# Kernel tuning notes

Measured on AMD Instinct MI355X. Metric: run time of the kernel, lower is better.

## Reference

```python
import jax, jax.numpy as jnp
import numpy as np

N = 50_000          # nodes
E = 1_600_000       # edges (avg degree 32)
F_IN = 8            # num_static_node_features
F_OUT = 12          # num_timesteps_in (TGCN hidden)
PERIODS = 6         # num_timesteps_out


def setup_inputs() -> dict:
    key = jax.random.key(0)
    ks = jax.random.split(key, 12)
    def n(k, shape, s=0.2):
        return jax.random.normal(k, shape, jnp.float32) * s
    return {
        "x": jax.random.normal(ks[0], (N, F_IN, PERIODS), jnp.float32),
        "edge_index": jax.random.randint(ks[1], (2, E), 0, N, dtype=jnp.int32),
        "edge_weight": jax.random.uniform(ks[2], (E,), jnp.float32),
        "att": n(ks[3], (PERIODS,), 1.0),
        "Wz": n(ks[4], (F_IN, F_OUT)), "bz": jnp.zeros((F_OUT,), jnp.float32),
        "Wr": n(ks[5], (F_IN, F_OUT)), "br": jnp.zeros((F_OUT,), jnp.float32),
        "Wh": n(ks[6], (F_IN, F_OUT)), "bh": jnp.zeros((F_OUT,), jnp.float32),
        "lzW": n(ks[7], (F_OUT, 2 * F_OUT)), "lzb": jnp.zeros((F_OUT,), jnp.float32),
        "lrW": n(ks[8], (F_OUT, 2 * F_OUT)), "lrb": jnp.zeros((F_OUT,), jnp.float32),
        "lhW": n(ks[9], (F_OUT, 2 * F_OUT)), "lhb": jnp.zeros((F_OUT,), jnp.float32),
        "linW": n(ks[10], (PERIODS, F_OUT)), "linb": jnp.zeros((PERIODS,), jnp.float32),
    }


def _gcn_norm(edge_index, edge_weight):
    # PyG gcn_norm: add self loops (weight 1.0), symmetric D^-1/2 A D^-1/2,
    # degree computed from dst (col) of edge_weight.
    src, dst = edge_index[0], edge_index[1]
    loop = jnp.arange(N, dtype=src.dtype)
    src = jnp.concatenate([src, loop])
    dst = jnp.concatenate([dst, loop])
    ew = jnp.concatenate([edge_weight, jnp.ones((N,), edge_weight.dtype)])
    deg = jax.ops.segment_sum(ew, dst, num_segments=N)
    dinv = jnp.where(deg > 0, 1.0 / jnp.sqrt(deg), 0.0)
    return src, dst, dinv[src] * ew * dinv[dst]


def _gcn_conv(xp, W, b, src, dst, norm):
    h = xp @ W                                  # [N, F_OUT]
    msg = norm[:, None] * h[src]                # gather over edges
    return jax.ops.segment_sum(msg, dst, num_segments=N) + b


def reference(x, edge_index, edge_weight, att, Wz, bz, Wr, br, Wh, bh,
              lzW, lzb, lrW, lrb, lhW, lhb, linW, linb):
    src, dst, norm = _gcn_norm(edge_index, edge_weight)
    H0 = jnp.zeros((N, F_OUT), x.dtype)  # A3TGCN passes H=None each period

    def tgcn_cell(xp):  # xp: [N, F_IN]
        Z = jax.nn.sigmoid(
            jnp.concatenate([_gcn_conv(xp, Wz, bz, src, dst, norm), H0], -1) @ lzW.T + lzb)
        R = jax.nn.sigmoid(
            jnp.concatenate([_gcn_conv(xp, Wr, br, src, dst, norm), H0], -1) @ lrW.T + lrb)
        Ht = jnp.tanh(
            jnp.concatenate([_gcn_conv(xp, Wh, bh, src, dst, norm), H0 * R], -1) @ lhW.T + lhb)
        return Z * H0 + (1.0 - Z) * Ht

    probs = jax.nn.softmax(att)                  # [P]
    Hs = jax.vmap(tgcn_cell, in_axes=2)(x)       # [P, N, F_OUT]
    H = jnp.einsum('p,pnf->nf', probs, Hs)       # attention-weighted sum
    h = jax.nn.relu(H)
    return h @ linW.T + linb                     # [N, PERIODS]
```

## Files before the change

### kernel.cpp

```cpp
#include <hip/hip_runtime.h>
#include <hip/hip_fp16.h>

#define N_NODES 50000
#define N_EDGES 1600000
#define F_IN 8
#define F_OUT 12
#define PERIODS 6
#define FP 48
#define BKT_SH 7
#define BKT_N 128
#define NBKT ((N_NODES + BKT_N - 1) / BKT_N)
#define CHK 4096
#define NCHK ((N_EDGES + CHK - 1) / CHK)
#define SEG_CAP 4736
#define SEG_AL  5120

typedef unsigned int u32x4 __attribute__((ext_vector_type(4)));

__global__ void k_zero(unsigned int* __restrict__ cursor) {
    int i = threadIdx.x;
    if (i < NBKT) cursor[i] = 0u;
}

__global__ void __launch_bounds__(1024) k_scatter(const int4* __restrict__ src4,
                                                  const int4* __restrict__ dst4,
                                                  const float4* __restrict__ ew4,
                                                  unsigned int* __restrict__ cursor,
                                                  unsigned long long* __restrict__ part) {
    __shared__ unsigned int h[NBKT];
    __shared__ unsigned int gbase[NBKT];
    int tid = threadIdx.x, blk = blockIdx.x;
    for (int k = tid; k < NBKT; k += 1024) h[k] = 0u;
    __syncthreads();
    int q = blk * 1024 + tid;
    bool v = (q < N_EDGES / 4);
    int4 ss = v ? src4[q] : make_int4(0, 0, 0, 0);
    int4 dd = v ? dst4[q] : make_int4(0, 0, 0, 0);
    float4 ww = v ? ew4[q] : make_float4(0.f, 0.f, 0.f, 0.f);
    int s[4] = { ss.x, ss.y, ss.z, ss.w };
    int d[4] = { dd.x, dd.y, dd.z, dd.w };
    float w[4] = { ww.x, ww.y, ww.z, ww.w };
    int bv[4]; unsigned int lr[4], lo[4], hiw[4];
    #pragma unroll
    for (int e = 0; e < 4; e++) {
        if (v) {
            int b = d[e] >> BKT_SH;
            bv[e] = b;
            lr[e] = atomicAdd(&h[b], 1u);
            lo[e] = ((unsigned int)(d[e] & (BKT_N - 1)) << 24) | (unsigned int)s[e];
            hiw[e] = __float_as_uint(w[e]);
        }
    }
    __syncthreads();
    for (int k = tid; k < NBKT; k += 1024) {
        unsigned int c = h[k];
        gbase[k] = c ? atomicAdd(&cursor[k], c) : 0u;
    }
    __syncthreads();
    if (v) {
        #pragma unroll
        for (int e = 0; e < 4; e++) {
            unsigned int off = gbase[bv[e]] + lr[e];
            if (off < SEG_CAP)
                part[(size_t)bv[e] * SEG_CAP + off] =
                    ((unsigned long long)hiw[e] << 32) | lo[e];
        }
    }
}

__global__ void __launch_bounds__(1024) k_bucket(const unsigned long long* __restrict__ part,
                                                 const unsigned int* __restrict__ cursor,
                                                 const float* __restrict__ x,
                                                 int2* __restrict__ offs2,
                                                 float* __restrict__ dinv_g,
                                                 uint4* __restrict__ xs,
                                                 unsigned int* __restrict__ csr4) {
    __shared__ uint2 stage[SEG_CAP];
    __shared__ unsigned int cnt[BKT_N], rowstart[BKT_N], sc[BKT_N];
    __shared__ float degf[BKT_N], dinv_l[BKT_N];
    int tid = threadIdx.x, k = blockIdx.x;
    unsigned int base = (unsigned int)k * SEG_CAP;
    unsigned int cbase = (unsigned int)k * SEG_AL;
    unsigned int m = cursor[k];
    if (m > SEG_CAP) m = SEG_CAP;
    if (tid < BKT_N) { cnt[tid] = 0u; degf[tid] = 1.0f; }
    __syncthreads();

    for (unsigned int i = tid; i < m; i += 1024) {
        unsigned long long p = __builtin_nontemporal_load(&part[base + i]);
        unsigned int lo = (unsigned int)p;
        unsigned int hi = (unsigned int)(p >> 32);
        unsigned int j = (lo >> 24) & (BKT_N - 1);
        unsigned int r = atomicAdd(&cnt[j], 1u);
        atomicAdd(&degf[j], __uint_as_float(hi));
        if (r > 255u) r = 255u;
        stage[i] = make_uint2(lo | (r << 16), hi);
    }
    __syncthreads();

    if (tid < 64) {
        unsigned int a = (cnt[tid] + 3u) & ~3u;
        unsigned int b = (cnt[tid + 64] + 3u) & ~3u;
        unsigned int sa = a;
        #pragma unroll
        for (int off = 1; off < 64; off <<= 1) {
            unsigned int tv = __shfl_up(sa, off);
            if ((tid & 63) >= off) sa += tv;
        }
        unsigned int tot = __shfl(sa, 63);
        unsigned int sb = b;
        #pragma unroll
        for (int off = 1; off < 64; off <<= 1) {
            unsigned int tv = __shfl_up(sb, off);
            if ((tid & 63) >= off) sb += tv;
        }
        sc[tid] = sa;
        sc[tid + 64] = sb + tot;
    }
    __syncthreads();

    int n0 = k * BKT_N;
    int nn = N_NODES - n0; if (nn > BKT_N) nn = BKT_N;

    if (tid < BKT_N) {
        unsigned int ca = (cnt[tid] + 3u) & ~3u;
        unsigned int rs = sc[tid] - ca;
        rowstart[tid] = rs;
        float dv = rsqrtf(degf[tid]);
        dinv_l[tid] = dv;
        if (tid < nn) {
            dinv_g[n0 + tid] = dv;
            offs2[n0 + tid] = make_int2((int)(cbase + rs),
                                        (int)(cbase + rs + cnt[tid]));
        }
    }
    __syncthreads();

    for (unsigned int i = tid; i < m; i += 1024) {
        uint2 vv = stage[i];
        unsigned int j = (vv.x >> 24) & (BKT_N - 1);
        unsigned int r = (vv.x >> 16) & 0xFFu;
        __half hw = __float2half(__uint_as_float(vv.y));
        unsigned int entry = ((unsigned int)__half_as_ushort(hw) << 16) |
                             (vv.x & 0xFFFFu);
        csr4[cbase + rowstart[j] + r] = entry;
    }

    for (int idx = tid; idx < nn * 6; idx += 1024) {
        int j = idx / 6, c = idx % 6;
        float di = dinv_l[j];
        const float4* xr = (const float4*)(x + (size_t)(n0 + j) * FP + c * 8);
        float4 a = xr[0], b = xr[1];
        __half2 h0 = __floats2half2_rn(di * a.x, di * a.y);
        __half2 h1 = __floats2half2_rn(di * a.z, di * a.w);
        __half2 h2 = __floats2half2_rn(di * b.x, di * b.y);
        __half2 h3 = __floats2half2_rn(di * b.z, di * b.w);
        uint4 o;
        o.x = *(unsigned int*)&h0; o.y = *(unsigned int*)&h1;
        o.z = *(unsigned int*)&h2; o.w = *(unsigned int*)&h3;
        xs[(size_t)(n0 + j) * 6 + c] = o;
    }
}

__global__ void __launch_bounds__(192) k_gnode(const uint4* __restrict__ xs,
                                               const float* __restrict__ dinv,
                                               const int2* __restrict__ offs2,
                                               const unsigned int* __restrict__ csr4,
                                               const float* __restrict__ att,
                                               const float* __restrict__ Wz,
                                               const float* __restrict__ bz,
                                               const float* __restrict__ Wh,
                                               const float* __restrict__ bh,
                                               const float* __restrict__ lzW,
                                               const float* __restrict__ lzb,
                                               const float* __restrict__ lhW,
                                               const float* __restrict__ lhb,
                                               const float* __restrict__ linW,
                                               const float* __restrict__ linb,
                                               float* __restrict__ out) {
    __shared__ float row[8][48];
    __shared__ float gzs[8][72];
    __shared__ float ghs[8][72];
    __shared__ float Hl[8][12];

    int tid = threadIdx.x;
    int L = tid / 24, r = tid % 24, c = r >> 2, g = r & 3;
    int n = blockIdx.x * 8 + L;

    int2 oe = offs2[n];
    const unsigned int* rowp = csr4 + oe.x;
    int cnt = oe.y - oe.x;
    float a0 = 0.f, a1 = 0.f, a2 = 0.f, a3 = 0.f;
    float a4 = 0.f, a5 = 0.f, a6 = 0.f, a7 = 0.f;
    int kk = 0;
    for (; kk + 16 <= cnt; kk += 16) {
        u32x4 pc = __builtin_nontemporal_load((const u32x4*)(rowp + kk + 4 * g));
        unsigned int p[4] = { pc.x, pc.y, pc.z, pc.w };
        uint4 v[4];
        #pragma unroll
        for (int u = 0; u < 4; u++)
            v[u] = xs[(size_t)(p[u] & 0xFFFFu) * 6 + c];
        #pragma unroll
        for (int u = 0; u < 4; u++) {
            float w = __half2float(__ushort_as_half((unsigned short)(p[u] >> 16)));
            float2 e0 = __half22float2(*(__half2*)&v[u].x);
            float2 e1 = __half22float2(*(__half2*)&v[u].y);
            float2 e2 = __half22float2(*(__half2*)&v[u].z);
            float2 e3 = __half22float2(*(__half2*)&v[u].w);
            a0 += w * e0.x; a1 += w * e0.y; a2 += w * e1.x; a3 += w * e1.y;
            a4 += w * e2.x; a5 += w * e2.y; a6 += w * e3.x; a7 += w * e3.y;
        }
    }
    int tlo = kk + 4 * g, thi = tlo + 4; if (thi > cnt) thi = cnt;
    for (int jj = tlo; jj < thi; jj++) {
        unsigned int p = __builtin_nontemporal_load(rowp + jj);
        float w = __half2float(__ushort_as_half((unsigned short)(p >> 16)));
        uint4 v = xs[(size_t)(p & 0xFFFFu) * 6 + c];
        float2 e0 = __half22float2(*(__half2*)&v.x);
        float2 e1 = __half22float2(*(__half2*)&v.y);
        float2 e2 = __half22float2(*(__half2*)&v.z);
        float2 e3 = __half22float2(*(__half2*)&v.w);
        a0 += w * e0.x; a1 += w * e0.y; a2 += w * e1.x; a3 += w * e1.y;
        a4 += w * e2.x; a5 += w * e2.y; a6 += w * e3.x; a7 += w * e3.y;
    }
    a0 += __shfl_xor(a0, 1); a1 += __shfl_xor(a1, 1);
    a2 += __shfl_xor(a2, 1); a3 += __shfl_xor(a3, 1);
    a4 += __shfl_xor(a4, 1); a5 += __shfl_xor(a5, 1);
    a6 += __shfl_xor(a6, 1); a7 += __shfl_xor(a7, 1);
    a0 += __shfl_xor(a0, 2); a1 += __shfl_xor(a1, 2);
    a2 += __shfl_xor(a2, 2); a3 += __shfl_xor(a3, 2);
    a4 += __shfl_xor(a4, 2); a5 += __shfl_xor(a5, 2);
    a6 += __shfl_xor(a6, 2); a7 += __shfl_xor(a7, 2);
    if (g == 0) {
        uint4 sf = xs[(size_t)n * 6 + c];
        float2 s0 = __half22float2(*(__half2*)&sf.x);
        float2 s1 = __half22float2(*(__half2*)&sf.y);
        float2 s2 = __half22float2(*(__half2*)&sf.z);
        float2 s3 = __half22float2(*(__half2*)&sf.w);
        float di = dinv[n];
        row[L][8 * c + 0] = di * (a0 + s0.x); row[L][8 * c + 1] = di * (a1 + s0.y);
        row[L][8 * c + 2] = di * (a2 + s1.x); row[L][8 * c + 3] = di * (a3 + s1.y);
        row[L][8 * c + 4] = di * (a4 + s2.x); row[L][8 * c + 5] = di * (a5 + s2.y);
        row[L][8 * c + 6] = di * (a6 + s3.x); row[L][8 * c + 7] = di * (a7 + s3.y);
    }
    __syncthreads();

    for (int it = r; it < 72; it += 24) {
        int p = it / 12, q = it - p * 12;
        float gz = bz[q], gh = bh[q];
        #pragma unroll
        for (int f = 0; f < F_IN; f++) {
            float xv = row[L][f * 6 + p];
            gz += xv * Wz[f * F_OUT + q];
            gh += xv * Wh[f * F_OUT + q];
        }
        gzs[L][it] = gz; ghs[L][it] = gh;
    }
    __syncthreads();

    if (r < 12) {
        float a[PERIODS];
        float mx = -1e30f;
        #pragma unroll
        for (int p = 0; p < PERIODS; p++) { a[p] = att[p]; mx = fmaxf(mx, a[p]); }
        float se = 0.f;
        #pragma unroll
        for (int p = 0; p < PERIODS; p++) { a[p] = __expf(a[p] - mx); se += a[p]; }
        float inv = 1.f / se;
        int j = r;
        float hacc = 0.f;
        #pragma unroll
        for (int p = 0; p < PERIODS; p++) {
            float z = lzb[j], t2 = lhb[j];
            #pragma unroll
            for (int q = 0; q < F_OUT; q++) {
                z  += gzs[L][p * 12 + q] * lzW[j * (2 * F_OUT) + q];
                t2 += ghs[L][p * 12 + q] * lhW[j * (2 * F_OUT) + q];
            }
            float Z = 1.f / (1.f + __expf(-z));
            float e2 = __expf(2.f * t2);
            float th = 1.f - __fdividef(2.f, e2 + 1.f);
            hacc += (a[p] * inv) * (1.f - Z) * th;
        }
        Hl[L][j] = fmaxf(hacc, 0.f);
    }
    __syncthreads();

    if (r < PERIODS) {
        float acc = linb[r];
        #pragma unroll
        for (int j = 0; j < F_OUT; j++)
            acc += Hl[L][j] * linW[r * F_OUT + j];
        out[(size_t)n * PERIODS + r] = acc;
    }
}

extern "C" void kernel_launch(void* const* d_in, const int* in_sizes, int n_in,
                              void* d_out, int out_size, void* d_ws, size_t ws_size,
                              hipStream_t stream) {
    const float* x    = (const float*)d_in[0];
    const int*   ei   = (const int*)d_in[1];
    const float* ew   = (const float*)d_in[2];
    const float* att  = (const float*)d_in[3];
    const float* Wz   = (const float*)d_in[4];
    const float* bz   = (const float*)d_in[5];
    const float* Wh   = (const float*)d_in[8];
    const float* bh   = (const float*)d_in[9];
    const float* lzW  = (const float*)d_in[10];
    const float* lzb  = (const float*)d_in[11];
    const float* lhW  = (const float*)d_in[14];
    const float* lhb  = (const float*)d_in[15];
    const float* linW = (const float*)d_in[16];
    const float* linb = (const float*)d_in[17];
    float* out = (float*)d_out;

    uint4* xs   = (uint4*)d_ws;
    unsigned long long* part = (unsigned long long*)(xs + (size_t)N_NODES * 6);
    unsigned int* csr4 = (unsigned int*)(part + (size_t)NBKT * SEG_CAP);
    int2*  offs2 = (int2*)(csr4 + (size_t)NBKT * SEG_AL);
    float* dinv  = (float*)(offs2 + N_NODES);
    unsigned int* cursor = (unsigned int*)(dinv + N_NODES);

    const int* srcp = ei;
    const int* dstp = ei + N_EDGES;

    k_zero<<<1, 512, 0, stream>>>(cursor);
    k_scatter<<<NCHK, 1024, 0, stream>>>((const int4*)srcp, (const int4*)dstp,
                                         (const float4*)ew, cursor, part);
    k_bucket<<<NBKT, 1024, 0, stream>>>(part, cursor, x, offs2, dinv, xs, csr4);
    k_gnode<<<N_NODES / 8, 192, 0, stream>>>(xs, dinv, offs2, csr4, att,
                                             Wz, bz, Wh, bh, lzW, lzb, lhW, lhb,
                                             linW, linb, out);
}
```

Baseline: 187.3 us.

## Replace CSR build with per-bucket LDS atomic aggregation fused with node epilogue

Drops the per-bucket CSR construction and the separate per-node gather kernel. Each bucket block now reads its partitioned edges directly and accumulates weighted neighbour features into shared memory with atomics, then runs the GRU/attention/linear epilogue for its 128 nodes in the same kernel. Degree is accumulated with global float atomics in the scatter kernel, and a small kernel builds the scaled half-precision features. The aim is to remove the CSR write/read pass and one launch. In exchange it adds heavy LDS atomic traffic (48 per edge), global atomics on degree, and only about 391 blocks for the main work.

```diff
diff --git a/kernel.cpp b/kernel.cpp
--- a/kernel.cpp
+++ b/kernel.cpp
@@ -13,19 +13,19 @@
 #define CHK 4096
 #define NCHK ((N_EDGES + CHK - 1) / CHK)
 #define SEG_CAP 4736
-#define SEG_AL  5120
-
-typedef unsigned int u32x4 __attribute__((ext_vector_type(4)));
-
-__global__ void k_zero(unsigned int* __restrict__ cursor) {
-    int i = threadIdx.x;
-    if (i < NBKT) cursor[i] = 0u;
+#define ACC_W 49
+
+__global__ void k_init(unsigned int* __restrict__ cursor, float* __restrict__ deg) {
+    int t = blockIdx.x * blockDim.x + threadIdx.x;
+    if (t < N_NODES) deg[t] = 1.0f;
+    if (t < NBKT) cursor[t] = 0u;
 }
 
 __global__ void __launch_bounds__(1024) k_scatter(const int4* __restrict__ src4,
                                                   const int4* __restrict__ dst4,
                                                   const float4* __restrict__ ew4,
                                                   unsigned int* __restrict__ cursor,
+                                                  float* __restrict__ deg,
                                                   unsigned long long* __restrict__ part) {
     __shared__ unsigned int h[NBKT];
     __shared__ unsigned int gbase[NBKT];
@@ -49,6 +49,7 @@
             lr[e] = atomicAdd(&h[b], 1u);
             lo[e] = ((unsigned int)(d[e] & (BKT_N - 1)) << 24) | (unsigned int)s[e];
             hiw[e] = __float_as_uint(w[e]);
+            atomicAdd(&deg[d[e]], w[e]);
         }
     }
     __syncthreads();
@@ -68,230 +69,161 @@
     }
 }
 
-__global__ void __launch_bounds__(1024) k_bucket(const unsigned long long* __restrict__ part,
-                                                 const unsigned int* __restrict__ cursor,
-                                                 const float* __restrict__ x,
-                                                 int2* __restrict__ offs2,
-                                                 float* __restrict__ dinv_g,
-                                                 uint4* __restrict__ xs,
-                                                 unsigned int* __restrict__ csr4) {
-    __shared__ uint2 stage[SEG_CAP];
-    __shared__ unsigned int cnt[BKT_N], rowstart[BKT_N], sc[BKT_N];
-    __shared__ float degf[BKT_N], dinv_l[BKT_N];
+__global__ void __launch_bounds__(256) k_xs(const float* __restrict__ x,
+                                            const float* __restrict__ deg,
+                                            float* __restrict__ dinv,
+                                            uint4* __restrict__ xs) {
+    int t = blockIdx.x * 256 + threadIdx.x;
+    if (t >= N_NODES * 6) return;
+    int n = t / 6, c = t % 6;
+    float di = rsqrtf(deg[n]);
+    if (c == 0) dinv[n] = di;
+    const float4* xr = (const float4*)(x + (size_t)n * FP + c * 8);
+    float4 a = xr[0], b = xr[1];
+    __half2 h0 = __floats2half2_rn(di * a.x, di * a.y);
+    __half2 h1 = __floats2half2_rn(di * a.z, di * a.w);
+    __half2 h2 = __floats2half2_rn(di * b.x, di * b.y);
+    __half2 h3 = __floats2half2_rn(di * b.z, di * b.w);
+    uint4 o;
+    o.x = *(unsigned int*)&h0; o.y = *(unsigned int*)&h1;
+    o.z = *(unsigned int*)&h2; o.w = *(unsigned int*)&h3;
+    xs[t] = o;
+}
+
+__global__ void __launch_bounds__(1024) k_bedge(const unsigned long long* __restrict__ part,
+                                                const unsigned int* __restrict__ cursor,
+                                                const uint4* __restrict__ xs,
+                                                const float* __restrict__ dinv,
+                                                const float* __restrict__ att,
+                                                const float* __restrict__ Wz,
+                                                const float* __restrict__ bz,
+                                                const float* __restrict__ Wh,
+                                                const float* __restrict__ bh,
+                                                const float* __restrict__ lzW,
+                                                const float* __restrict__ lzb,
+                                                const float* __restrict__ lhW,
+                                                const float* __restrict__ lhb,
+                                                const float* __restrict__ linW,
+                                                const float* __restrict__ linb,
+                                                float* __restrict__ out) {
+    __shared__ float acc[BKT_N * ACC_W];
+    __shared__ float Hl[BKT_N * F_OUT];
+    __shared__ float dinv_l[BKT_N];
+
     int tid = threadIdx.x, k = blockIdx.x;
+    int n0 = k * BKT_N;
+    int nn = N_NODES - n0; if (nn > BKT_N) nn = BKT_N;
     unsigned int base = (unsigned int)k * SEG_CAP;
-    unsigned int cbase = (unsigned int)k * SEG_AL;
     unsigned int m = cursor[k];
     if (m > SEG_CAP) m = SEG_CAP;
-    if (tid < BKT_N) { cnt[tid] = 0u; degf[tid] = 1.0f; }
-    __syncthreads();
-
-    for (unsigned int i = tid; i < m; i += 1024) {
-        unsigned long long p = __builtin_nontemporal_load(&part[base + i]);
-        unsigned int lo = (unsigned int)p;
-        unsigned int hi = (unsigned int)(p >> 32);
-        unsigned int j = (lo >> 24) & (BKT_N - 1);
-        unsigned int r = atomicAdd(&cnt[j], 1u);
-        atomicAdd(&degf[j], __uint_as_float(hi));
-        if (r > 255u) r = 255u;
-        stage[i] = make_uint2(lo | (r << 16), hi);
-    }
-    __syncthreads();
-
-    if (tid < 64) {
-        unsigned int a = (cnt[tid] + 3u) & ~3u;
-        unsigned int b = (cnt[tid + 64] + 3u) & ~3u;
-        unsigned int sa = a;
-        #pragma unroll
-        for (int off = 1; off < 64; off <<= 1) {
-            unsigned int tv = __shfl_up(sa, off);
-            if ((tid & 63) >= off) sa += tv;
-        }
-        unsigned int tot = __shfl(sa, 63);
-        unsigned int sb = b;
-        #pragma unroll
-        for (int off = 1; off < 64; off <<= 1) {
-            unsigned int tv = __shfl_up(sb, off);
-            if ((tid & 63) >= off) sb += tv;
-        }
-        sc[tid] = sa;
-        sc[tid + 64] = sb + tot;
-    }
-    __syncthreads();
-
-    int n0 = k * BKT_N;
-    int nn = N_NODES - n0; if (nn > BKT_N) nn = BKT_N;
-
-    if (tid < BKT_N) {
-        unsigned int ca = (cnt[tid] + 3u) & ~3u;
-        unsigned int rs = sc[tid] - ca;
-        rowstart[tid] = rs;
-        float dv = rsqrtf(degf[tid]);
-        dinv_l[tid] = dv;
-        if (tid < nn) {
-            dinv_g[n0 + tid] = dv;
-            offs2[n0 + tid] = make_int2((int)(cbase + rs),
-                                        (int)(cbase + rs + cnt[tid]));
-        }
-    }
-    __syncthreads();
-
-    for (unsigned int i = tid; i < m; i += 1024) {
-        uint2 vv = stage[i];
-        unsigned int j = (vv.x >> 24) & (BKT_N - 1);
-        unsigned int r = (vv.x >> 16) & 0xFFu;
-        __half hw = __float2half(__uint_as_float(vv.y));
-        unsigned int entry = ((unsigned int)__half_as_ushort(hw) << 16) |
-                             (vv.x & 0xFFFFu);
-        csr4[cbase + rowstart[j] + r] = entry;
-    }
-
-    for (int idx = tid; idx < nn * 6; idx += 1024) {
-        int j = idx / 6, c = idx % 6;
-        float di = dinv_l[j];
-        const float4* xr = (const float4*)(x + (size_t)(n0 + j) * FP + c * 8);
-        float4 a = xr[0], b = xr[1];
-        __half2 h0 = __floats2half2_rn(di * a.x, di * a.y);
-        __half2 h1 = __floats2half2_rn(di * a.z, di * a.w);
-        __half2 h2 = __floats2half2_rn(di * b.x, di * b.y);
-        __half2 h3 = __floats2half2_rn(di * b.z, di * b.w);
-        uint4 o;
-        o.x = *(unsigned int*)&h0; o.y = *(unsigned int*)&h1;
-        o.z = *(unsigned int*)&h2; o.w = *(unsigned int*)&h3;
-        xs[(size_t)(n0 + j) * 6 + c] = o;
-    }
-}
-
-__global__ void __launch_bounds__(192) k_gnode(const uint4* __restrict__ xs,
-                                               const float* __restrict__ dinv,
-                                               const int2* __restrict__ offs2,
-                                               const unsigned int* __restrict__ csr4,
-                                               const float* __restrict__ att,
-                                               const float* __restrict__ Wz,
-                                               const float* __restrict__ bz,
-                                               const float* __restrict__ Wh,
-                                               const float* __restrict__ bh,
-                                               const float* __restrict__ lzW,
-                                               const float* __restrict__ lzb,
-                                               const float* __restrict__ lhW,
-                                               const float* __restrict__ lhb,
-                                               const float* __restrict__ linW,
-                                               const float* __restrict__ linb,
-                                               float* __restrict__ out) {
-    __shared__ float row[8][48];
-    __shared__ float gzs[8][72];
-    __shared__ float ghs[8][72];
-    __shared__ float Hl[8][12];
-
-    int tid = threadIdx.x;
-    int L = tid / 24, r = tid % 24, c = r >> 2, g = r & 3;
-    int n = blockIdx.x * 8 + L;
-
-    int2 oe = offs2[n];
-    const unsigned int* rowp = csr4 + oe.x;
-    int cnt = oe.y - oe.x;
-    float a0 = 0.f, a1 = 0.f, a2 = 0.f, a3 = 0.f;
-    float a4 = 0.f, a5 = 0.f, a6 = 0.f, a7 = 0.f;
-    int kk = 0;
-    for (; kk + 16 <= cnt; kk += 16) {
-        u32x4 pc = __builtin_nontemporal_load((const u32x4*)(rowp + kk + 4 * g));
-        unsigned int p[4] = { pc.x, pc.y, pc.z, pc.w };
-        uint4 v[4];
-        #pragma unroll
-        for (int u = 0; u < 4; u++)
-            v[u] = xs[(size_t)(p[u] & 0xFFFFu) * 6 + c];
-        #pragma unroll
-        for (int u = 0; u < 4; u++) {
-            float w = __half2float(__ushort_as_half((unsigned short)(p[u] >> 16)));
-            float2 e0 = __half22float2(*(__half2*)&v[u].x);
-            float2 e1 = __half22float2(*(__half2*)&v[u].y);
-            float2 e2 = __half22float2(*(__half2*)&v[u].z);
-            float2 e3 = __half22float2(*(__half2*)&v[u].w);
-            a0 += w * e0.x; a1 += w * e0.y; a2 += w * e1.x; a3 += w * e1.y;
-            a4 += w * e2.x; a5 += w * e2.y; a6 += w * e3.x; a7 += w * e3.y;
-        }
-    }
-    int tlo = kk + 4 * g, thi = tlo + 4; if (thi > cnt) thi = cnt;
-    for (int jj = tlo; jj < thi; jj++) {
-        unsigned int p = __builtin_nontemporal_load(rowp + jj);
-        float w = __half2float(__ushort_as_half((unsigned short)(p >> 16)));
-        uint4 v = xs[(size_t)(p & 0xFFFFu) * 6 + c];
-        float2 e0 = __half22float2(*(__half2*)&v.x);
-        float2 e1 = __half22float2(*(__half2*)&v.y);
-        float2 e2 = __half22float2(*(__half2*)&v.z);
-        float2 e3 = __half22float2(*(__half2*)&v.w);
-        a0 += w * e0.x; a1 += w * e0.y; a2 += w * e1.x; a3 += w * e1.y;
-        a4 += w * e2.x; a5 += w * e2.y; a6 += w * e3.x; a7 += w * e3.y;
-    }
-    a0 += __shfl_xor(a0, 1); a1 += __shfl_xor(a1, 1);
-    a2 += __shfl_xor(a2, 1); a3 += __shfl_xor(a3, 1);
-    a4 += __shfl_xor(a4, 1); a5 += __shfl_xor(a5, 1);
-    a6 += __shfl_xor(a6, 1); a7 += __shfl_xor(a7, 1);
-    a0 += __shfl_xor(a0, 2); a1 += __shfl_xor(a1, 2);
-    a2 += __shfl_xor(a2, 2); a3 += __shfl_xor(a3, 2);
-    a4 += __shfl_xor(a4, 2); a5 += __shfl_xor(a5, 2);
-    a6 += __shfl_xor(a6, 2); a7 += __shfl_xor(a7, 2);
-    if (g == 0) {
-        uint4 sf = xs[(size_t)n * 6 + c];
-        float2 s0 = __half22float2(*(__half2*)&sf.x);
-        float2 s1 = __half22float2(*(__half2*)&sf.y);
-        float2 s2 = __half22float2(*(__half2*)&sf.z);
-        float2 s3 = __half22float2(*(__half2*)&sf.w);
-        float di = dinv[n];
-        row[L][8 * c + 0] = di * (a0 + s0.x); row[L][8 * c + 1] = di * (a1 + s0.y);
-        row[L][8 * c + 2] = di * (a2 + s1.x); row[L][8 * c + 3] = di * (a3 + s1.y);
-        row[L][8 * c + 4] = di * (a4 + s2.x); row[L][8 * c + 5] = di * (a5 + s2.y);
-        row[L][8 * c + 6] = di * (a6 + s3.x); row[L][8 * c + 7] = di * (a7 + s3.y);
-    }
-    __syncthreads();
-
-    for (int it = r; it < 72; it += 24) {
-        int p = it / 12, q = it - p * 12;
-        float gz = bz[q], gh = bh[q];
-        #pragma unroll
-        for (int f = 0; f < F_IN; f++) {
-            float xv = row[L][f * 6 + p];
-            gz += xv * Wz[f * F_OUT + q];
-            gh += xv * Wh[f * F_OUT + q];
-        }
-        gzs[L][it] = gz; ghs[L][it] = gh;
-    }
-    __syncthreads();
-
-    if (r < 12) {
-        float a[PERIODS];
-        float mx = -1e30f;
-        #pragma unroll
-        for (int p = 0; p < PERIODS; p++) { a[p] = att[p]; mx = fmaxf(mx, a[p]); }
-        float se = 0.f;
-        #pragma unroll
-        for (int p = 0; p < PERIODS; p++) { a[p] = __expf(a[p] - mx); se += a[p]; }
-        float inv = 1.f / se;
-        int j = r;
-        float hacc = 0.f;
-        #pragma unroll
-        for (int p = 0; p < PERIODS; p++) {
-            float z = lzb[j], t2 = lhb[j];
-            #pragma unroll
-            for (int q = 0; q < F_OUT; q++) {
-                z  += gzs[L][p * 12 + q] * lzW[j * (2 * F_OUT) + q];
-                t2 += ghs[L][p * 12 + q] * lhW[j * (2 * F_OUT) + q];
-            }
-            float Z = 1.f / (1.f + __expf(-z));
-            float e2 = __expf(2.f * t2);
-            float th = 1.f - __fdividef(2.f, e2 + 1.f);
-            hacc += (a[p] * inv) * (1.f - Z) * th;
-        }
-        Hl[L][j] = fmaxf(hacc, 0.f);
-    }
-    __syncthreads();
-
-    if (r < PERIODS) {
-        float acc = linb[r];
-        #pragma unroll
-        for (int j = 0; j < F_OUT; j++)
-            acc += Hl[L][j] * linW[r * F_OUT + j];
-        out[(size_t)n * PERIODS + r] = acc;
+
+    for (int i = tid; i < BKT_N * ACC_W; i += 1024) acc[i] = 0.f;
+    for (int i = tid; i < BKT_N * F_OUT; i += 1024) Hl[i] = 0.f;
+    if (tid < nn) dinv_l[tid] = dinv[n0 + tid];
+    __syncthreads();
+
+    {
+        int grp = tid >> 1, kk = tid & 1;
+        for (unsigned int e = grp; e < m; e += 512) {
+            unsigned long long pe = __builtin_nontemporal_load(&part[base + e]);
+            unsigned int lo = (unsigned int)pe;
+            float w = __uint_as_float((unsigned int)(pe >> 32));
+            int src = (int)(lo & 0xFFFFu);
+            int dl  = (int)((lo >> 24) & (BKT_N - 1));
+            float* arow = acc + dl * ACC_W;
+            #pragma unroll
+            for (int u = 0; u < 3; u++) {
+                int c = kk + 2 * u;
+                uint4 vv = xs[(size_t)src * 6 + c];
+                float2 e0 = __half22float2(*(__half2*)&vv.x);
+                float2 e1 = __half22float2(*(__half2*)&vv.y);
+                float2 e2 = __half22float2(*(__half2*)&vv.z);
+                float2 e3 = __half22float2(*(__half2*)&vv.w);
+                float* ap = arow + 8 * c;
+                atomicAdd(&ap[0], w * e0.x); atomicAdd(&ap[1], w * e0.y);
+                atomicAdd(&ap[2], w * e1.x); atomicAdd(&ap[3], w * e1.y);
+                atomicAdd(&ap[4], w * e2.x); atomicAdd(&ap[5], w * e2.y);
+                atomicAdd(&ap[6], w * e3.x); atomicAdd(&ap[7], w * e3.y);
+            }
+        }
+    }
+    __syncthreads();
+
+    if (tid < BKT_N * 6) {
+        int j = tid / 6, c = tid % 6;
+        if (j < nn) {
+            uint4 vv = xs[(size_t)(n0 + j) * 6 + c];
+            float dv = dinv_l[j];
+            float2 e0 = __half22float2(*(__half2*)&vv.x);
+            float2 e1 = __half22float2(*(__half2*)&vv.y);
+            float2 e2 = __half22float2(*(__half2*)&vv.z);
+            float2 e3 = __half22float2(*(__half2*)&vv.w);
+            float* ap = acc + j * ACC_W + 8 * c;
+            ap[0] = dv * (ap[0] + e0.x); ap[1] = dv * (ap[1] + e0.y);
+            ap[2] = dv * (ap[2] + e1.x); ap[3] = dv * (ap[3] + e1.y);
+            ap[4] = dv * (ap[4] + e2.x); ap[5] = dv * (ap[5] + e2.y);
+            ap[6] = dv * (ap[6] + e3.x); ap[7] = dv * (ap[7] + e3.y);
+        }
+    }
+    __syncthreads();
+
+    if (tid < PERIODS * BKT_N) {
+        int p = tid >> 7, jn = tid & (BKT_N - 1);
+        if (jn < nn) {
+            float mx = -1e30f;
+            #pragma unroll
+            for (int pp = 0; pp < PERIODS; pp++) mx = fmaxf(mx, att[pp]);
+            float se = 0.f, ap = 0.f;
+            #pragma unroll
+            for (int pp = 0; pp < PERIODS; pp++) {
+                float ev = __expf(att[pp] - mx);
+                se += ev;
+                if (pp == p) ap = ev;
+            }
+            ap /= se;
+
+            float rv[F_IN];
+            #pragma unroll
+            for (int f = 0; f < F_IN; f++) rv[f] = acc[jn * ACC_W + f * 6 + p];
+
+            float gz[F_OUT], gh[F_OUT];
+            #pragma unroll
+            for (int q = 0; q < F_OUT; q++) { gz[q] = bz[q]; gh[q] = bh[q]; }
+            #pragma unroll
+            for (int f = 0; f < F_IN; f++) {
+                float xv = rv[f];
+                #pragma unroll
+                for (int q = 0; q < F_OUT; q++) {
+                    gz[q] += xv * Wz[f * F_OUT + q];
+                    gh[q] += xv * Wh[f * F_OUT + q];
+                }
+            }
+            #pragma unroll
+            for (int j = 0; j < F_OUT; j++) {
+                float z = lzb[j], t2 = lhb[j];
+                #pragma unroll
+                for (int q = 0; q < F_OUT; q++) {
+                    z  += gz[q] * lzW[j * (2 * F_OUT) + q];
+                    t2 += gh[q] * lhW[j * (2 * F_OUT) + q];
+                }
+                float Z = 1.f / (1.f + __expf(-z));
+                float e2 = __expf(2.f * t2);
+                float th = 1.f - __fdividef(2.f, e2 + 1.f);
+                atomicAdd(&Hl[jn * F_OUT + j], ap * (1.f - Z) * th);
+            }
+        }
+    }
+    __syncthreads();
+
+    if (tid < BKT_N * PERIODS) {
+        int jn = tid / PERIODS, q = tid % PERIODS;
+        if (jn < nn) {
+            float a2 = linb[q];
+            #pragma unroll
+            for (int j = 0; j < F_OUT; j++)
+                a2 += fmaxf(Hl[jn * F_OUT + j], 0.f) * linW[q * F_OUT + j];
+            out[(size_t)(n0 + jn) * PERIODS + q] = a2;
+        }
     }
 }
 
@@ -316,19 +248,18 @@
 
     uint4* xs   = (uint4*)d_ws;
     unsigned long long* part = (unsigned long long*)(xs + (size_t)N_NODES * 6);
-    unsigned int* csr4 = (unsigned int*)(part + (size_t)NBKT * SEG_CAP);
-    int2*  offs2 = (int2*)(csr4 + (size_t)NBKT * SEG_AL);
-    float* dinv  = (float*)(offs2 + N_NODES);
+    float* deg  = (float*)(part + (size_t)NBKT * SEG_CAP);
+    float* dinv = deg + N_NODES;
     unsigned int* cursor = (unsigned int*)(dinv + N_NODES);
 
     const int* srcp = ei;
     const int* dstp = ei + N_EDGES;
 
-    k_zero<<<1, 512, 0, stream>>>(cursor);
+    k_init<<<(N_NODES + 1023) / 1024, 1024, 0, stream>>>(cursor, deg);
     k_scatter<<<NCHK, 1024, 0, stream>>>((const int4*)srcp, (const int4*)dstp,
-                                         (const float4*)ew, cursor, part);
-    k_bucket<<<NBKT, 1024, 0, stream>>>(part, cursor, x, offs2, dinv, xs, csr4);
-    k_gnode<<<N_NODES / 8, 192, 0, stream>>>(xs, dinv, offs2, csr4, att,
-                                             Wz, bz, Wh, bh, lzW, lzb, lhW, lhb,
-                                             linW, linb, out);
-}
+                                         (const float4*)ew, cursor, deg, part);
+    k_xs<<<(N_NODES * 6 + 255) / 256, 256, 0, stream>>>(x, deg, dinv, xs);
+    k_bedge<<<NBKT, 1024, 0, stream>>>(part, cursor, xs, dinv, att,
+                                       Wz, bz, Wh, bh, lzW, lzb, lhW, lhb,
+                                       linW, linb, out);
+}
```

After: 731.7 us. 291% more time.

## Fuse CSR bucket build with neighbor gather and move degree to scatter atomics

Applied to the files above, without the earlier changes.

Degree accumulation moves out of the bucket kernel into global fixed-point atomics during the edge scatter. A new elementwise kernel then computes dinv and the scaled half-precision node features up front. The bucket kernel is merged with the per-node gather and GRU/attention epilogue, so each 128-node bucket builds its CSR segment in LDS and consumes it immediately. This removes the offs2 array and one launch, but it costs 1.6M random global atomics, a large LDS footprint, and only ~391 blocks doing the latency-bound gather.

```diff
diff --git a/kernel.cpp b/kernel.cpp
--- a/kernel.cpp
+++ b/kernel.cpp
@@ -14,18 +14,22 @@
 #define NCHK ((N_EDGES + CHK - 1) / CHK)
 #define SEG_CAP 4736
 #define SEG_AL  5120
+#define DEG_SCALE 16777216.0f
+#define DEG_INV  5.9604644775390625e-8f
 
 typedef unsigned int u32x4 __attribute__((ext_vector_type(4)));
 
-__global__ void k_zero(unsigned int* __restrict__ cursor) {
-    int i = threadIdx.x;
-    if (i < NBKT) cursor[i] = 0u;
+__global__ void k_init(unsigned int* __restrict__ cursor, unsigned int* __restrict__ degu) {
+    int t = blockIdx.x * blockDim.x + threadIdx.x;
+    if (t < N_NODES) degu[t] = 1u << 24;
+    if (t < NBKT) cursor[t] = 0u;
 }
 
 __global__ void __launch_bounds__(1024) k_scatter(const int4* __restrict__ src4,
                                                   const int4* __restrict__ dst4,
                                                   const float4* __restrict__ ew4,
                                                   unsigned int* __restrict__ cursor,
+                                                  unsigned int* __restrict__ degu,
                                                   unsigned long long* __restrict__ part) {
     __shared__ unsigned int h[NBKT];
     __shared__ unsigned int gbase[NBKT];
@@ -49,6 +53,7 @@
             lr[e] = atomicAdd(&h[b], 1u);
             lo[e] = ((unsigned int)(d[e] & (BKT_N - 1)) << 24) | (unsigned int)s[e];
             hiw[e] = __float_as_uint(w[e]);
+            atomicAdd(&degu[d[e]], __float2uint_rn(w[e] * DEG_SCALE));
         }
     }
     __syncthreads();
@@ -68,22 +73,66 @@
     }
 }
 
-__global__ void __launch_bounds__(1024) k_bucket(const unsigned long long* __restrict__ part,
-                                                 const unsigned int* __restrict__ cursor,
-                                                 const float* __restrict__ x,
-                                                 int2* __restrict__ offs2,
-                                                 float* __restrict__ dinv_g,
-                                                 uint4* __restrict__ xs,
-                                                 unsigned int* __restrict__ csr4) {
-    __shared__ uint2 stage[SEG_CAP];
+__global__ void __launch_bounds__(256) k_xs(const float* __restrict__ x,
+                                            const unsigned int* __restrict__ degu,
+                                            float* __restrict__ dinv,
+                                            uint4* __restrict__ xs) {
+    int t = blockIdx.x * 256 + threadIdx.x;
+    if (t >= N_NODES * 6) return;
+    int n = t / 6, c = t % 6;
+    float di = rsqrtf((float)degu[n] * DEG_INV);
+    if (c == 0) dinv[n] = di;
+    const float4* xr = (const float4*)(x + (size_t)n * FP + c * 8);
+    float4 a = xr[0], b = xr[1];
+    __half2 h0 = __floats2half2_rn(di * a.x, di * a.y);
+    __half2 h1 = __floats2half2_rn(di * a.z, di * a.w);
+    __half2 h2 = __floats2half2_rn(di * b.x, di * b.y);
+    __half2 h3 = __floats2half2_rn(di * b.z, di * b.w);
+    uint4 o;
+    o.x = *(unsigned int*)&h0; o.y = *(unsigned int*)&h1;
+    o.z = *(unsigned int*)&h2; o.w = *(unsigned int*)&h3;
+    xs[t] = o;
+}
+
+__global__ void __launch_bounds__(1024) k_bgn(const unsigned long long* __restrict__ part,
+                                              const unsigned int* __restrict__ cursor,
+                                              const uint4* __restrict__ xs,
+                                              const float* __restrict__ dinv,
+                                              unsigned int* __restrict__ csr4,
+                                              const float* __restrict__ att,
+                                              const float* __restrict__ Wz,
+                                              const float* __restrict__ bz,
+                                              const float* __restrict__ Wh,
+                                              const float* __restrict__ bh,
+                                              const float* __restrict__ lzW,
+                                              const float* __restrict__ lzb,
+                                              const float* __restrict__ lhW,
+                                              const float* __restrict__ lhb,
+                                              const float* __restrict__ linW,
+                                              const float* __restrict__ linb,
+                                              float* __restrict__ out) {
+    __shared__ union {
+        uint2 stage[SEG_CAP];
+        struct {
+            float row[BKT_N][48];
+            float Hl[BKT_N][F_OUT];
+        } e;
+    } u;
+    __shared__ float gzs[64][72], ghs[64][72];
     __shared__ unsigned int cnt[BKT_N], rowstart[BKT_N], sc[BKT_N];
-    __shared__ float degf[BKT_N], dinv_l[BKT_N];
+    __shared__ float dinv_l[BKT_N];
+
     int tid = threadIdx.x, k = blockIdx.x;
+    int n0 = k * BKT_N;
+    int nn = N_NODES - n0; if (nn > BKT_N) nn = BKT_N;
     unsigned int base = (unsigned int)k * SEG_CAP;
     unsigned int cbase = (unsigned int)k * SEG_AL;
     unsigned int m = cursor[k];
     if (m > SEG_CAP) m = SEG_CAP;
-    if (tid < BKT_N) { cnt[tid] = 0u; degf[tid] = 1.0f; }
+    if (tid < BKT_N) {
+        cnt[tid] = 0u;
+        dinv_l[tid] = (tid < nn) ? dinv[n0 + tid] : 0.f;
+    }
     __syncthreads();
 
     for (unsigned int i = tid; i < m; i += 1024) {
@@ -92,9 +141,8 @@
         unsigned int hi = (unsigned int)(p >> 32);
         unsigned int j = (lo >> 24) & (BKT_N - 1);
         unsigned int r = atomicAdd(&cnt[j], 1u);
-        atomicAdd(&degf[j], __uint_as_float(hi));
         if (r > 255u) r = 255u;
-        stage[i] = make_uint2(lo | (r << 16), hi);
+        u.stage[i] = make_uint2(lo | (r << 16), hi);
     }
     __syncthreads();
 
@@ -118,26 +166,14 @@
         sc[tid + 64] = sb + tot;
     }
     __syncthreads();
-
-    int n0 = k * BKT_N;
-    int nn = N_NODES - n0; if (nn > BKT_N) nn = BKT_N;
-
     if (tid < BKT_N) {
         unsigned int ca = (cnt[tid] + 3u) & ~3u;
-        unsigned int rs = sc[tid] - ca;
-        rowstart[tid] = rs;
-        float dv = rsqrtf(degf[tid]);
-        dinv_l[tid] = dv;
-        if (tid < nn) {
-            dinv_g[n0 + tid] = dv;
-            offs2[n0 + tid] = make_int2((int)(cbase + rs),
-                                        (int)(cbase + rs + cnt[tid]));
-        }
+        rowstart[tid] = sc[tid] - ca;
     }
     __syncthreads();
 
     for (unsigned int i = tid; i < m; i += 1024) {
-        uint2 vv = stage[i];
+        uint2 vv = u.stage[i];
         unsigned int j = (vv.x >> 24) & (BKT_N - 1);
         unsigned int r = (vv.x >> 16) & 0xFFu;
         __half hw = __float2half(__uint_as_float(vv.y));
@@ -145,153 +181,126 @@
                              (vv.x & 0xFFFFu);
         csr4[cbase + rowstart[j] + r] = entry;
     }
-
-    for (int idx = tid; idx < nn * 6; idx += 1024) {
-        int j = idx / 6, c = idx % 6;
-        float di = dinv_l[j];
-        const float4* xr = (const float4*)(x + (size_t)(n0 + j) * FP + c * 8);
-        float4 a = xr[0], b = xr[1];
-        __half2 h0 = __floats2half2_rn(di * a.x, di * a.y);
-        __half2 h1 = __floats2half2_rn(di * a.z, di * a.w);
-        __half2 h2 = __floats2half2_rn(di * b.x, di * b.y);
-        __half2 h3 = __floats2half2_rn(di * b.z, di * b.w);
-        uint4 o;
-        o.x = *(unsigned int*)&h0; o.y = *(unsigned int*)&h1;
-        o.z = *(unsigned int*)&h2; o.w = *(unsigned int*)&h3;
-        xs[(size_t)(n0 + j) * 6 + c] = o;
-    }
-}
-
-__global__ void __launch_bounds__(192) k_gnode(const uint4* __restrict__ xs,
-                                               const float* __restrict__ dinv,
-                                               const int2* __restrict__ offs2,
-                                               const unsigned int* __restrict__ csr4,
-                                               const float* __restrict__ att,
-                                               const float* __restrict__ Wz,
-                                               const float* __restrict__ bz,
-                                               const float* __restrict__ Wh,
-                                               const float* __restrict__ bh,
-                                               const float* __restrict__ lzW,
-                                               const float* __restrict__ lzb,
-                                               const float* __restrict__ lhW,
-                                               const float* __restrict__ lhb,
-                                               const float* __restrict__ linW,
-                                               const float* __restrict__ linb,
-                                               float* __restrict__ out) {
-    __shared__ float row[8][48];
-    __shared__ float gzs[8][72];
-    __shared__ float ghs[8][72];
-    __shared__ float Hl[8][12];
-
-    int tid = threadIdx.x;
-    int L = tid / 24, r = tid % 24, c = r >> 2, g = r & 3;
-    int n = blockIdx.x * 8 + L;
-
-    int2 oe = offs2[n];
-    const unsigned int* rowp = csr4 + oe.x;
-    int cnt = oe.y - oe.x;
-    float a0 = 0.f, a1 = 0.f, a2 = 0.f, a3 = 0.f;
-    float a4 = 0.f, a5 = 0.f, a6 = 0.f, a7 = 0.f;
-    int kk = 0;
-    for (; kk + 16 <= cnt; kk += 16) {
-        u32x4 pc = __builtin_nontemporal_load((const u32x4*)(rowp + kk + 4 * g));
-        unsigned int p[4] = { pc.x, pc.y, pc.z, pc.w };
-        uint4 v[4];
-        #pragma unroll
-        for (int u = 0; u < 4; u++)
-            v[u] = xs[(size_t)(p[u] & 0xFFFFu) * 6 + c];
-        #pragma unroll
-        for (int u = 0; u < 4; u++) {
-            float w = __half2float(__ushort_as_half((unsigned short)(p[u] >> 16)));
-            float2 e0 = __half22float2(*(__half2*)&v[u].x);
-            float2 e1 = __half22float2(*(__half2*)&v[u].y);
-            float2 e2 = __half22float2(*(__half2*)&v[u].z);
-            float2 e3 = __half22float2(*(__half2*)&v[u].w);
+    __syncthreads();
+
+    for (int P = 0; P < 3; P++) {
+        int rr = P * 1024 + tid;
+        int nL = rr / 24, lane = rr % 24, c = lane >> 2, g = lane & 3;
+        const unsigned int* rowp = csr4 + cbase + rowstart[nL];
+        int cntv = (int)cnt[nL];
+        float a0 = 0.f, a1 = 0.f, a2 = 0.f, a3 = 0.f;
+        float a4 = 0.f, a5 = 0.f, a6 = 0.f, a7 = 0.f;
+        int kk = 0;
+        for (; kk + 16 <= cntv; kk += 16) {
+            u32x4 pc = __builtin_nontemporal_load((const u32x4*)(rowp + kk + 4 * g));
+            unsigned int p[4] = { pc.x, pc.y, pc.z, pc.w };
+            uint4 v[4];
+            #pragma unroll
+            for (int uu = 0; uu < 4; uu++)
+                v[uu] = xs[(size_t)(p[uu] & 0xFFFFu) * 6 + c];
+            #pragma unroll
+            for (int uu = 0; uu < 4; uu++) {
+                float w = __half2float(__ushort_as_half((unsigned short)(p[uu] >> 16)));
+                float2 e0 = __half22float2(*(__half2*)&v[uu].x);
+                float2 e1 = __half22float2(*(__half2*)&v[uu].y);
+                float2 e2 = __half22float2(*(__half2*)&v[uu].z);
+                float2 e3 = __half22float2(*(__half2*)&v[uu].w);
+                a0 += w * e0.x; a1 += w * e0.y; a2 += w * e1.x; a3 += w * e1.y;
+                a4 += w * e2.x; a5 += w * e2.y; a6 += w * e3.x; a7 += w * e3.y;
+            }
+        }
+        int tlo = kk + 4 * g, thi = tlo + 4; if (thi > cntv) thi = cntv;
+        for (int jj = tlo; jj < thi; jj++) {
+            unsigned int p = __builtin_nontemporal_load(rowp + jj);
+            float w = __half2float(__ushort_as_half((unsigned short)(p >> 16)));
+            uint4 v = xs[(size_t)(p & 0xFFFFu) * 6 + c];
+            float2 e0 = __half22float2(*(__half2*)&v.x);
+            float2 e1 = __half22float2(*(__half2*)&v.y);
+            float2 e2 = __half22float2(*(__half2*)&v.z);
+            float2 e3 = __half22float2(*(__half2*)&v.w);
             a0 += w * e0.x; a1 += w * e0.y; a2 += w * e1.x; a3 += w * e1.y;
             a4 += w * e2.x; a5 += w * e2.y; a6 += w * e3.x; a7 += w * e3.y;
         }
-    }
-    int tlo = kk + 4 * g, thi = tlo + 4; if (thi > cnt) thi = cnt;
-    for (int jj = tlo; jj < thi; jj++) {
-        unsigned int p = __builtin_nontemporal_load(rowp + jj);
-        float w = __half2float(__ushort_as_half((unsigned short)(p >> 16)));
-        uint4 v = xs[(size_t)(p & 0xFFFFu) * 6 + c];
-        float2 e0 = __half22float2(*(__half2*)&v.x);
-        float2 e1 = __half22float2(*(__half2*)&v.y);
-        float2 e2 = __half22float2(*(__half2*)&v.z);
-        float2 e3 = __half22float2(*(__half2*)&v.w);
-        a0 += w * e0.x; a1 += w * e0.y; a2 += w * e1.x; a3 += w * e1.y;
-        a4 += w * e2.x; a5 += w * e2.y; a6 += w * e3.x; a7 += w * e3.y;
-    }
-    a0 += __shfl_xor(a0, 1); a1 += __shfl_xor(a1, 1);
-    a2 += __shfl_xor(a2, 1); a3 += __shfl_xor(a3, 1);
-    a4 += __shfl_xor(a4, 1); a5 += __shfl_xor(a5, 1);
-    a6 += __shfl_xor(a6, 1); a7 += __shfl_xor(a7, 1);
-    a0 += __shfl_xor(a0, 2); a1 += __shfl_xor(a1, 2);
-    a2 += __shfl_xor(a2, 2); a3 += __shfl_xor(a3, 2);
-    a4 += __shfl_xor(a4, 2); a5 += __shfl_xor(a5, 2);
-    a6 += __shfl_xor(a6, 2); a7 += __shfl_xor(a7, 2);
-    if (g == 0) {
-        uint4 sf = xs[(size_t)n * 6 + c];
-        float2 s0 = __half22float2(*(__half2*)&sf.x);
-        float2 s1 = __half22float2(*(__half2*)&sf.y);
-        float2 s2 = __half22float2(*(__half2*)&sf.z);
-        float2 s3 = __half22float2(*(__half2*)&sf.w);
-        float di = dinv[n];
-        row[L][8 * c + 0] = di * (a0 + s0.x); row[L][8 * c + 1] = di * (a1 + s0.y);
-        row[L][8 * c + 2] = di * (a2 + s1.x); row[L][8 * c + 3] = di * (a3 + s1.y);
-        row[L][8 * c + 4] = di * (a4 + s2.x); row[L][8 * c + 5] = di * (a5 + s2.y);
-        row[L][8 * c + 6] = di * (a6 + s3.x); row[L][8 * c + 7] = di * (a7 + s3.y);
-    }
-    __syncthreads();
-
-    for (int it = r; it < 72; it += 24) {
-        int p = it / 12, q = it - p * 12;
-        float gz = bz[q], gh = bh[q];
-        #pragma unroll
-        for (int f = 0; f < F_IN; f++) {
-            float xv = row[L][f * 6 + p];
-            gz += xv * Wz[f * F_OUT + q];
-            gh += xv * Wh[f * F_OUT + q];
-        }
-        gzs[L][it] = gz; ghs[L][it] = gh;
-    }
-    __syncthreads();
-
-    if (r < 12) {
-        float a[PERIODS];
-        float mx = -1e30f;
-        #pragma unroll
-        for (int p = 0; p < PERIODS; p++) { a[p] = att[p]; mx = fmaxf(mx, a[p]); }
-        float se = 0.f;
-        #pragma unroll
-        for (int p = 0; p < PERIODS; p++) { a[p] = __expf(a[p] - mx); se += a[p]; }
-        float inv = 1.f / se;
-        int j = r;
-        float hacc = 0.f;
-        #pragma unroll
-        for (int p = 0; p < PERIODS; p++) {
-            float z = lzb[j], t2 = lhb[j];
-            #pragma unroll
-            for (int q = 0; q < F_OUT; q++) {
-                z  += gzs[L][p * 12 + q] * lzW[j * (2 * F_OUT) + q];
-                t2 += ghs[L][p * 12 + q] * lhW[j * (2 * F_OUT) + q];
+        a0 += __shfl_xor(a0, 1); a1 += __shfl_xor(a1, 1);
+        a2 += __shfl_xor(a2, 1); a3 += __shfl_xor(a3, 1);
+        a4 += __shfl_xor(a4, 1); a5 += __shfl_xor(a5, 1);
+        a6 += __shfl_xor(a6, 1); a7 += __shfl_xor(a7, 1);
+        a0 += __shfl_xor(a0, 2); a1 += __shfl_xor(a1, 2);
+        a2 += __shfl_xor(a2, 2); a3 += __shfl_xor(a3, 2);
+        a4 += __shfl_xor(a4, 2); a5 += __shfl_xor(a5, 2);
+        a6 += __shfl_xor(a6, 2); a7 += __shfl_xor(a7, 2);
+        if (g == 0 && nL < nn) {
+            uint4 sf = xs[(size_t)(n0 + nL) * 6 + c];
+            float2 s0 = __half22float2(*(__half2*)&sf.x);
+            float2 s1 = __half22float2(*(__half2*)&sf.y);
+            float2 s2 = __half22float2(*(__half2*)&sf.z);
+            float2 s3 = __half22float2(*(__half2*)&sf.w);
+            float dv = dinv_l[nL];
+            u.e.row[nL][8 * c + 0] = dv * (a0 + s0.x);
+            u.e.row[nL][8 * c + 1] = dv * (a1 + s0.y);
+            u.e.row[nL][8 * c + 2] = dv * (a2 + s1.x);
+            u.e.row[nL][8 * c + 3] = dv * (a3 + s1.y);
+            u.e.row[nL][8 * c + 4] = dv * (a4 + s2.x);
+            u.e.row[nL][8 * c + 5] = dv * (a5 + s2.y);
+            u.e.row[nL][8 * c + 6] = dv * (a6 + s3.x);
+            u.e.row[nL][8 * c + 7] = dv * (a7 + s3.y);
+        }
+    }
+    __syncthreads();
+
+    for (int h = 0; h < 2; h++) {
+        int nb = h * 64;
+        for (int it = tid; it < 64 * 72; it += 1024) {
+            int jn = it / 72, pq = it - jn * 72;
+            int p = pq / 12, q = pq - p * 12;
+            float gz = bz[q], gh = bh[q];
+            #pragma unroll
+            for (int f = 0; f < F_IN; f++) {
+                float xv = u.e.row[nb + jn][f * 6 + p];
+                gz += xv * Wz[f * F_OUT + q];
+                gh += xv * Wh[f * F_OUT + q];
             }
-            float Z = 1.f / (1.f + __expf(-z));
-            float e2 = __expf(2.f * t2);
-            float th = 1.f - __fdividef(2.f, e2 + 1.f);
-            hacc += (a[p] * inv) * (1.f - Z) * th;
-        }
-        Hl[L][j] = fmaxf(hacc, 0.f);
-    }
-    __syncthreads();
-
-    if (r < PERIODS) {
-        float acc = linb[r];
-        #pragma unroll
-        for (int j = 0; j < F_OUT; j++)
-            acc += Hl[L][j] * linW[r * F_OUT + j];
-        out[(size_t)n * PERIODS + r] = acc;
+            gzs[jn][pq] = gz; ghs[jn][pq] = gh;
+        }
+        __syncthreads();
+        if (tid < 64 * 12) {
+            int jn = tid / 12, j = tid - jn * 12;
+            float a[PERIODS];
+            float mx = -1e30f;
+            #pragma unroll
+            for (int p = 0; p < PERIODS; p++) { a[p] = att[p]; mx = fmaxf(mx, a[p]); }
+            float se = 0.f;
+            #pragma unroll
+            for (int p = 0; p < PERIODS; p++) { a[p] = __expf(a[p] - mx); se += a[p]; }
+            float inv = 1.f / se;
+            float hacc = 0.f;
+            #pragma unroll
+            for (int p = 0; p < PERIODS; p++) {
+                float z = lzb[j], t2 = lhb[j];
+                #pragma unroll
+                for (int q = 0; q < F_OUT; q++) {
+                    z  += gzs[jn][p * 12 + q] * lzW[j * (2 * F_OUT) + q];
+                    t2 += ghs[jn][p * 12 + q] * lhW[j * (2 * F_OUT) + q];
+                }
+                float Z = 1.f / (1.f + __expf(-z));
+                float e2 = __expf(2.f * t2);
+                float th = 1.f - __fdividef(2.f, e2 + 1.f);
+                hacc += (a[p] * inv) * (1.f - Z) * th;
+            }
+            u.e.Hl[nb + jn][j] = fmaxf(hacc, 0.f);
+        }
+        __syncthreads();
+    }
+
+    if (tid < BKT_N * PERIODS) {
+        int jn = tid / PERIODS, q = tid - jn * PERIODS;
+        if (jn < nn) {
+            float acc = linb[q];
+            #pragma unroll
+            for (int j = 0; j < F_OUT; j++)
+                acc += u.e.Hl[jn][j] * linW[q * F_OUT + j];
+            out[(size_t)(n0 + jn) * PERIODS + q] = acc;
+        }
     }
 }
 
@@ -317,18 +326,18 @@
     uint4* xs   = (uint4*)d_ws;
     unsigned long long* part = (unsigned long long*)(xs + (size_t)N_NODES * 6);
     unsigned int* csr4 = (unsigned int*)(part + (size_t)NBKT * SEG_CAP);
-    int2*  offs2 = (int2*)(csr4 + (size_t)NBKT * SEG_AL);
-    float* dinv  = (float*)(offs2 + N_NODES);
+    unsigned int* degu = csr4 + (size_t)NBKT * SEG_AL;
+    float* dinv = (float*)(degu + N_NODES);
     unsigned int* cursor = (unsigned int*)(dinv + N_NODES);
 
     const int* srcp = ei;
     const int* dstp = ei + N_EDGES;
 
-    k_zero<<<1, 512, 0, stream>>>(cursor);
+    k_init<<<(N_NODES + 1023) / 1024, 1024, 0, stream>>>(cursor, degu);
     k_scatter<<<NCHK, 1024, 0, stream>>>((const int4*)srcp, (const int4*)dstp,
-                                         (const float4*)ew, cursor, part);
-    k_bucket<<<NBKT, 1024, 0, stream>>>(part, cursor, x, offs2, dinv, xs, csr4);
-    k_gnode<<<N_NODES / 8, 192, 0, stream>>>(xs, dinv, offs2, csr4, att,
-                                             Wz, bz, Wh, bh, lzW, lzb, lhW, lhb,
-                                             linW, linb, out);
-}
+                                         (const float4*)ew, cursor, degu, part);
+    k_xs<<<(N_NODES * 6 + 255) / 256, 256, 0, stream>>>(x, degu, dinv, xs);
+    k_bgn<<<NBKT, 1024, 0, stream>>>(part, cursor, xs, dinv, csr4, att,
+                                     Wz, bz, Wh, bh, lzW, lzb, lhW, lhb,
+                                     linW, linb, out);
+}
```

Measured after the change: 256.0 us. 36.7% more time.
